# Kernel optimization log

Measured on AMD Instinct MI355X. Metric: run time of the kernel, lower is better.

The kernel has to match this reference:

```python
import jax, jax.numpy as jnp
import numpy as np

B, S, N, HID = 4, 512, 128, 64


def setup_inputs() -> dict:
    key = jax.random.key(0)
    ks = jax.random.split(key, 32)
    def rn(k, shape, scale=0.1):
        return jax.random.normal(k, shape, dtype=jnp.float32) * scale
    adj = jax.random.randint(ks[0], (N, N), 0, 2).astype(jnp.int32)
    adj = adj.at[jnp.arange(N), jnp.arange(N)].set(1)  # self loops
    inp = {
        'x': jax.random.normal(ks[1], (B, S, N, 1), dtype=jnp.float32),
        'adj': adj,
        'emb_w': rn(ks[2], (1, 16)), 'emb_b': jnp.zeros((16,), jnp.float32),
        'gat1_W': rn(ks[3], (16, 16)), 'gat1_a': rn(ks[4], (32, 1)),
        'gat2_W': rn(ks[5], (16, 8)), 'gat2_a': rn(ks[6], (16, 1)),
        'Wih0': rn(ks[7], (4 * HID, N)), 'Whh0': rn(ks[8], (4 * HID, HID)),
        'bih0': jnp.zeros((4 * HID,), jnp.float32), 'bhh0': jnp.zeros((4 * HID,), jnp.float32),
        'Wih1': rn(ks[9], (4 * HID, HID)), 'Whh1': rn(ks[10], (4 * HID, HID)),
        'bih1': jnp.zeros((4 * HID,), jnp.float32), 'bhh1': jnp.zeros((4 * HID,), jnp.float32),
    }
    comb = HID + 8 * N
    for i, name in enumerate(['dir', 'ret', 'vol']):
        o = 2 if name == 'vol' else 1
        inp[name + '_w1'] = rn(ks[11 + 4 * i], (comb, 32))
        inp[name + '_b1'] = jnp.zeros((32,), jnp.float32)
        inp[name + '_w2'] = rn(ks[12 + 4 * i], (32, o))
        inp[name + '_b2'] = jnp.zeros((o,), jnp.float32)
    return inp


def _gat(h, W, a, mask):
    # e_ij = leakyrelu(a1 . Wh_i + a2 . Wh_j): avoid torch's [M,N,N,2F] concat.
    Wh = h @ W                                  # [M, N, F]
    Fo = W.shape[1]
    f1 = Wh @ a[:Fo]                            # [M, N, 1]
    f2 = Wh @ a[Fo:]                            # [M, N, 1]
    e = jax.nn.leaky_relu(f1 + jnp.swapaxes(f2, 1, 2), 0.2)  # [M, N, N]
    e = jnp.where(mask, e, jnp.float32(-9e15))
    attn = jax.nn.softmax(e, axis=2)
    return attn @ Wh                            # [M, N, F]


def _lstm_layer(xs, Wih, Whh, bih, bhh):
    # xs: [S, B, I]; PyTorch gate order i, f, g, o
    Bsz = xs.shape[1]
    Hd = Whh.shape[1]
    def step(carry, xt):
        h, c = carry
        g = xt @ Wih.T + h @ Whh.T + bih + bhh
        i, f, gg, o = jnp.split(g, 4, axis=-1)
        c = jax.nn.sigmoid(f) * c + jax.nn.sigmoid(i) * jnp.tanh(gg)
        h = jax.nn.sigmoid(o) * jnp.tanh(c)
        return (h, c), h
    init = (jnp.zeros((Bsz, Hd), xs.dtype), jnp.zeros((Bsz, Hd), xs.dtype))
    _, hs = jax.lax.scan(step, init, xs)
    return hs


def reference(x, adj, emb_w, emb_b, gat1_W, gat1_a, gat2_W, gat2_a,
              Wih0, Whh0, bih0, bhh0, Wih1, Whh1, bih1, bhh1,
              dir_w1, dir_b1, dir_w2, dir_b2,
              ret_w1, ret_b1, ret_w2, ret_b2,
              vol_w1, vol_b1, vol_w2, vol_b2):
    Bz, Sz, Nz, _ = x.shape
    mask = (adj > 0)[None]                      # [1, N, N], broadcast over B*S
    xe = (x @ emb_w + emb_b).reshape(Bz * Sz, Nz, 16)
    xg = jax.nn.elu(_gat(xe, gat1_W, gat1_a, mask))   # gat1 concat=True -> elu
    xg = _gat(xg, gat2_W, gat2_a, mask)               # gat2 concat=False
    xg_out = xg.reshape(Bz, Sz, Nz * 8)[:, -1, :]
    xs = jnp.swapaxes(x.reshape(Bz, Sz, Nz), 0, 1)    # [S, B, N]
    hs = _lstm_layer(xs, Wih0, Whh0, bih0, bhh0)
    hs = _lstm_layer(hs, Wih1, Whh1, bih1, bhh1)      # inter-layer dropout off (eval)
    xl_out = hs[-1]                                   # [B, 64]
    c = jnp.concatenate([xl_out, xg_out], axis=1)     # [B, 64 + 8N]
    def head(w1, b1, w2, b2):
        return jax.nn.relu(c @ w1 + b1) @ w2 + b2
    return (head(dir_w1, dir_b1, dir_w2, dir_b2),
            head(ret_w1, ret_b1, ret_w2, ret_b2),
            head(vol_w1, vol_b1, vol_w2, vol_b2))
```

## Files before the change

kernel.cpp:

```cpp
#include <hip/hip_runtime.h>

#define SEQ   512
#define BATCH 4
#define NN    128
#define HID   64
#define G4    256

__device__ __forceinline__ float frcp(float x)  { return __builtin_amdgcn_rcpf(x); }
__device__ __forceinline__ float fsigm(float x) { return frcp(1.f + __expf(-x)); }
__device__ __forceinline__ float ftanh(float x) { return 1.f - 2.f * frcp(1.f + __expf(2.f * x)); }
__device__ __forceinline__ float lrelu(float x) { return x > 0.f ? x : 0.2f * x; }
__device__ __forceinline__ float dot4f(float4 w, float4 h) {
  return fmaf(w.x, h.x, fmaf(w.y, h.y, fmaf(w.z, h.z, w.w * h.w)));
}
__device__ __forceinline__ void pin4(float4& v) {
  asm volatile("" : "+v"(v.x), "+v"(v.y), "+v"(v.z), "+v"(v.w));
}
__device__ __forceinline__ float qsum(float x) {
  x += __int_as_float(__builtin_amdgcn_update_dpp(
      0, __float_as_int(x), 0xB1, 0xF, 0xF, true));
  x += __int_as_float(__builtin_amdgcn_update_dpp(
      0, __float_as_int(x), 0x4E, 0xF, 0xF, true));
  return x;
}
__device__ __forceinline__ float dotacc(const float4* w, const float4* h, float a) {
#pragma unroll
  for (int c = 0; c < 4; ++c) {
    a = fmaf(w[c].x, h[c].x, a);
    a = fmaf(w[c].y, h[c].y, a);
    a = fmaf(w[c].z, h[c].z, a);
    a = fmaf(w[c].w, h[c].w, a);
  }
  return a;
}

__global__ __launch_bounds__(512) void prep_kernel(
    const float* __restrict__ x, const float* __restrict__ Wih0,
    const float* __restrict__ bih0, const float* __restrict__ bhh0,
    float* __restrict__ X0,
    const int* __restrict__ adj, const float* __restrict__ emb_w,
    const float* __restrict__ emb_b,
    const float* __restrict__ W1, const float* __restrict__ a1,
    const float* __restrict__ W2, const float* __restrict__ a2,
    float* __restrict__ xg_out)
{
  const int tid = threadIdx.x;
  if (blockIdx.x < 128) {
    __shared__ __align__(16) float xls[NN];
    const int g = tid >> 1, half = tid & 1;
    float4 w4[16];
    {
      const float4* wp = reinterpret_cast<const float4*>(Wih0 + g * NN + half * 64);
#pragma unroll
      for (int i = 0; i < 16; ++i) w4[i] = wp[i];
    }
    const float bsum = bih0[g] + bhh0[g];
    const int r0 = blockIdx.x * 16;
    for (int r = r0; r < r0 + 16; ++r) {
      const int tt = r >> 2, b = r & 3;
      if (tid < NN) xls[tid] = x[(b * SEQ + tt) * NN + tid];
      __syncthreads();
      const float4* hp = reinterpret_cast<const float4*>(&xls[half * 64]);
      float p0 = 0.f, p1 = 0.f, p2 = 0.f, p3 = 0.f;
#pragma unroll
      for (int k = 0; k < 16; k += 4) {
        p0 += dot4f(w4[k],     hp[k]);
        p1 += dot4f(w4[k + 1], hp[k + 1]);
        p2 += dot4f(w4[k + 2], hp[k + 2]);
        p3 += dot4f(w4[k + 3], hp[k + 3]);
      }
      float p = (p0 + p1) + (p2 + p3);
      p += __shfl_xor(p, 1);
      if (half == 0) X0[r * G4 + (g & 63) * 4 + (g >> 6)] = p + bsum;
      __syncthreads();
    }
    return;
  }
  const int b = blockIdx.x - 128;
  __shared__ float adjm[NN * 129];
  __shared__ __align__(16) float xls[NN];
  __shared__ float u[16], v[16];
  __shared__ float Wh2[NN][9];
  __shared__ float f1b[NN], f2b[NN];
  __shared__ float p[NN];

  for (int idx = tid; idx < NN * NN; idx += 512)
    adjm[(idx >> 7) * 129 + (idx & 127)] = (adj[idx] > 0) ? 1.f : 0.f;
  if (tid < NN) xls[tid] = x[(b * SEQ + (SEQ - 1)) * NN + tid];
  if (tid < 16) {
    float uu = 0.f, vv = 0.f;
    for (int fp = 0; fp < 16; ++fp) {
      uu += emb_w[fp] * W1[fp * 16 + tid];
      vv += emb_b[fp] * W1[fp * 16 + tid];
    }
    u[tid] = uu; v[tid] = vv;
  }
  __syncthreads();
  float s1 = 0.f, t1 = 0.f, s2 = 0.f, t2 = 0.f;
  for (int f = 0; f < 16; ++f) {
    s1 += u[f] * a1[f];      t1 += v[f] * a1[f];
    s2 += u[f] * a1[16 + f]; t2 += v[f] * a1[16 + f];
  }
  if (tid < NN) {
    const int i = tid;
    const float f1i = xls[i] * s1 + t1;
    float m = -1e30f;
    for (int j = 0; j < NN; ++j)
      if (adjm[i * 129 + j] != 0.f)
        m = fmaxf(m, lrelu(f1i + xls[j] * s2 + t2));
    float ssum = 0.f, ps = 0.f;
    for (int j = 0; j < NN; ++j)
      if (adjm[i * 129 + j] != 0.f) {
        const float wgt = __expf(lrelu(f1i + xls[j] * s2 + t2) - m);
        ssum += wgt; ps += wgt * xls[j];
      }
    p[i] = ps / ssum;
  }
  __syncthreads();
  if (tid < NN) {
    const int i = tid;
    float xg1[16];
#pragma unroll
    for (int f = 0; f < 16; ++f) {
      const float ov = p[i] * u[f] + v[f];
      xg1[f] = ov > 0.f ? ov : expm1f(ov);
    }
    float wrow[8];
#pragma unroll
    for (int f2 = 0; f2 < 8; ++f2) wrow[f2] = 0.f;
#pragma unroll
    for (int f = 0; f < 16; ++f) {
      const float xv = xg1[f];
#pragma unroll
      for (int f2 = 0; f2 < 8; ++f2) wrow[f2] += xv * W2[f * 8 + f2];
    }
    float fb1 = 0.f, fb2 = 0.f;
#pragma unroll
    for (int f2 = 0; f2 < 8; ++f2) {
      Wh2[i][f2] = wrow[f2];
      fb1 += wrow[f2] * a2[f2];
      fb2 += wrow[f2] * a2[8 + f2];
    }
    f1b[i] = fb1; f2b[i] = fb2;
  }
  __syncthreads();
  if (tid < NN) {
    const int i = tid;
    const float fi = f1b[i];
    float m = -1e30f;
    for (int j = 0; j < NN; ++j)
      if (adjm[i * 129 + j] != 0.f)
        m = fmaxf(m, lrelu(fi + f2b[j]));
    float ssum = 0.f;
    float o[8];
#pragma unroll
    for (int f2 = 0; f2 < 8; ++f2) o[f2] = 0.f;
    for (int j = 0; j < NN; ++j)
      if (adjm[i * 129 + j] != 0.f) {
        const float wgt = __expf(lrelu(fi + f2b[j]) - m);
        ssum += wgt;
#pragma unroll
        for (int f2 = 0; f2 < 8; ++f2) o[f2] += wgt * Wh2[j][f2];
      }
    const float inv = 1.f / ssum;
#pragma unroll
    for (int f2 = 0; f2 < 8; ++f2)
      xg_out[b * (NN * 8) + i * 8 + f2] = o[f2] * inv;
  }
}

__global__ __attribute__((amdgpu_flat_work_group_size(768, 768),
                          amdgpu_waves_per_eu(3, 3)))
void lstm_heads(
    const float* __restrict__ X0T, const float* __restrict__ Whh0,
    const float* __restrict__ Wih1, const float* __restrict__ Whh1,
    const float* __restrict__ bih1, const float* __restrict__ bhh1,
    const float* __restrict__ xg,
    const float* __restrict__ dw1, const float* __restrict__ db1,
    const float* __restrict__ dw2, const float* __restrict__ db2,
    const float* __restrict__ rw1, const float* __restrict__ rb1,
    const float* __restrict__ rw2, const float* __restrict__ rb2,
    const float* __restrict__ vw1, const float* __restrict__ vb1,
    const float* __restrict__ vw2, const float* __restrict__ vb2,
    float* __restrict__ out)
{
  const int b   = blockIdx.x;
  const int t   = threadIdx.x;
  const int grp = t >> 8;
  const int r   = t & 255;
  const int uu  = r >> 2, q2 = r & 3;

  __shared__ __align__(16) float hb[2][2][HID];
  __shared__ __align__(16) float P1[2][G4];
  __shared__ float cbuf[1088];
  __shared__ float hidc[96];

  const float* Wsrc = (grp == 0) ? Whh0 : (grp == 1) ? Wih1 : Whh1;
  float4 w[4][4];
#pragma unroll
  for (int j = 0; j < 4; ++j) {
    const int row = (uu + 64 * j) * HID + 16 * q2;
#pragma unroll
    for (int c = 0; c < 4; ++c)
      w[j][c] = *reinterpret_cast<const float4*>(Wsrc + row + 4 * c);
    pin4(w[j][0]); pin4(w[j][1]); pin4(w[j][2]); pin4(w[j][3]);
  }
  float4 b1v = make_float4(0.f, 0.f, 0.f, 0.f);
  if (grp == 2) {
    b1v.x = bih1[uu]       + bhh1[uu];
    b1v.y = bih1[uu + 64]  + bhh1[uu + 64];
    b1v.z = bih1[uu + 128] + bhh1[uu + 128];
    b1v.w = bih1[uu + 192] + bhh1[uu + 192];
  }

  if (t < 256) reinterpret_cast<float*>(hb)[t] = 0.f;
  float cst = 0.f;
  const float* X0b = X0T + b * G4 + uu * 4;
  float4 cur = make_float4(0.f, 0.f, 0.f, 0.f);
  if (grp == 0) cur = *reinterpret_cast<const float4*>(X0b);
  __syncthreads();

#define LSTM_STEP(TT, RB, WB)                                                  \
  do {                                                                         \
    const float4* hp = reinterpret_cast<const float4*>(                        \
        (grp == 2) ? &hb[RB][1][0] : &hb[RB][0][0]);                           \
    float4 hq[4];                                                              \
    hq[0] = hp[4 * q2 + 0]; hq[1] = hp[4 * q2 + 1];                            \
    hq[2] = hp[4 * q2 + 2]; hq[3] = hp[4 * q2 + 3];                            \
    float4 p1v = make_float4(0.f, 0.f, 0.f, 0.f);                              \
    if (grp == 2) p1v = *reinterpret_cast<const float4*>(&P1[1 - (RB)][uu * 4]); \
    float4 nxt = cur;                                                          \
    if (grp == 0 && (TT) + 1 < SEQ)                                            \
      nxt = *reinterpret_cast<const float4*>(X0b + ((TT) + 1) * (BATCH * G4)); \
    float A0 = dotacc(w[0], hq, 0.f);                                          \
    float A1 = dotacc(w[1], hq, 0.f);                                          \
    float A2 = dotacc(w[2], hq, 0.f);                                          \
    float A3 = dotacc(w[3], hq, 0.f);                                          \
    const float S0 = qsum(A0), S1 = qsum(A1), S2 = qsum(A2), S3 = qsum(A3);    \
    if (grp == 0) {                                                            \
      if ((TT) < SEQ) {                                                        \
        const float gi = fsigm(S0 + cur.x);                                    \
        const float gf = fsigm(S1 + cur.y);                                    \
        const float gg = ftanh(S2 + cur.z);                                    \
        const float go = fsigm(S3 + cur.w);                                    \
        cst = fmaf(gf, cst, gi * gg);                                          \
        if (q2 == 0) hb[WB][0][uu] = go * ftanh(cst);                          \
      }                                                                        \
    } else if (grp == 1) {                                                     \
      if ((TT) >= 1 && (TT) <= SEQ) {                                          \
        const float sel = (q2 == 0) ? S0 : (q2 == 1) ? S1 : (q2 == 2) ? S2 : S3; \
        P1[RB][r] = sel;                                                       \
      }                                                                        \
    } else {                                                                   \
      if ((TT) >= 2) {                                                         \
        const float gi = fsigm(S0 + p1v.x + b1v.x);                            \
        const float gf = fsigm(S1 + p1v.y + b1v.y);                            \
        const float gg = ftanh(S2 + p1v.z + b1v.z);                            \
        const float go = fsigm(S3 + p1v.w + b1v.w);                            \
        cst = fmaf(gf, cst, gi * gg);                                          \
        if (q2 == 0) hb[WB][1][uu] = go * ftanh(cst);                          \
      }                                                                        \
    }                                                                          \
    cur = nxt;                                                                 \
    __syncthreads();                                                           \
  } while (0)

  for (int tt = 0; tt < SEQ + 2; tt += 2) {
    LSTM_STEP(tt, 0, 1);
    LSTM_STEP(tt + 1, 1, 0);
  }
#undef LSTM_STEP

  if (t < 64) cbuf[t] = hb[0][1][t];
  for (int k = t; k < 1024; k += 768) cbuf[64 + k] = xg[b * 1024 + k];
  __syncthreads();
  if (t < 96) {
    const int head = t >> 5, h = t & 31;
    const float* w1 = (head == 0) ? dw1 : (head == 1) ? rw1 : vw1;
    const float* b1 = (head == 0) ? db1 : (head == 1) ? rb1 : vb1;
    float a0 = 0.f, a1v = 0.f, a2v = 0.f, a3v = 0.f;
    for (int k = 0; k < 1088; k += 4) {
      a0  = fmaf(cbuf[k],     w1[k * 32 + h],       a0);
      a1v = fmaf(cbuf[k + 1], w1[(k + 1) * 32 + h], a1v);
      a2v = fmaf(cbuf[k + 2], w1[(k + 2) * 32 + h], a2v);
      a3v = fmaf(cbuf[k + 3], w1[(k + 3) * 32 + h], a3v);
    }
    hidc[head * 32 + h] = fmaxf(b1[h] + ((a0 + a1v) + (a2v + a3v)), 0.f);
  }
  __syncthreads();
  if (t < 4) {
    const int head2 = (t < 2) ? t : 2;
    const int o = (t < 2) ? 0 : (t - 2);
    const int odim = (t < 2) ? 1 : 2;
    const float* w2  = (head2 == 0) ? dw2 : (head2 == 1) ? rw2 : vw2;
    const float* b2p = (head2 == 0) ? db2 : (head2 == 1) ? rb2 : vb2;
    float acc = b2p[o];
    for (int hh = 0; hh < 32; ++hh)
      acc = fmaf(hidc[head2 * 32 + hh], w2[hh * odim + o], acc);
    const int off = (t == 0) ? b : (t == 1) ? (4 + b) : (8 + 2 * b + o);
    out[off] = acc;
  }
}

extern "C" void kernel_launch(void* const* d_in, const int* in_sizes, int n_in,
                              void* d_out, int out_size, void* d_ws, size_t ws_size,
                              hipStream_t stream) {
  const float* x     = (const float*)d_in[0];
  const int*   adj   = (const int*)  d_in[1];
  const float* emb_w = (const float*)d_in[2];
  const float* emb_b = (const float*)d_in[3];
  const float* g1W   = (const float*)d_in[4];
  const float* g1a   = (const float*)d_in[5];
  const float* g2W   = (const float*)d_in[6];
  const float* g2a   = (const float*)d_in[7];
  const float* Wih0  = (const float*)d_in[8];
  const float* Whh0  = (const float*)d_in[9];
  const float* bih0  = (const float*)d_in[10];
  const float* bhh0  = (const float*)d_in[11];
  const float* Wih1  = (const float*)d_in[12];
  const float* Whh1  = (const float*)d_in[13];
  const float* bih1  = (const float*)d_in[14];
  const float* bhh1  = (const float*)d_in[15];
  const float* dw1 = (const float*)d_in[16]; const float* db1 = (const float*)d_in[17];
  const float* dw2 = (const float*)d_in[18]; const float* db2 = (const float*)d_in[19];
  const float* rw1 = (const float*)d_in[20]; const float* rb1 = (const float*)d_in[21];
  const float* rw2 = (const float*)d_in[22]; const float* rb2 = (const float*)d_in[23];
  const float* vw1 = (const float*)d_in[24]; const float* vb1 = (const float*)d_in[25];
  const float* vw2 = (const float*)d_in[26]; const float* vb2 = (const float*)d_in[27];

  float* ws = (float*)d_ws;
  float* X0 = ws;
  float* xg = ws + SEQ * BATCH * G4;
  float* out = (float*)d_out;

  hipLaunchKernelGGL(prep_kernel, dim3(132), dim3(512), 0, stream,
                     x, Wih0, bih0, bhh0, X0,
                     adj, emb_w, emb_b, g1W, g1a, g2W, g2a, xg);
  hipLaunchKernelGGL(lstm_heads, dim3(BATCH), dim3(768), 0, stream,
                     X0, Whh0, Wih1, Whh1, bih1, bhh1, xg,
                     dw1, db1, dw2, db2, rw1, rb1, rw2, rb2,
                     vw1, vb1, vw2, vb2, out);
}
```

Before: 469.6 us.

## Merge layer-1 input and recurrent projections into one thread group

```diff
diff --git a/kernel.cpp b/kernel.cpp
--- a/kernel.cpp
+++ b/kernel.cpp
@@ -169,8 +169,8 @@
   }
 }
 
-__global__ __attribute__((amdgpu_flat_work_group_size(768, 768),
-                          amdgpu_waves_per_eu(3, 3)))
+__global__ __attribute__((amdgpu_flat_work_group_size(512, 512),
+                          amdgpu_waves_per_eu(2, 2)))
 void lstm_heads(
     const float* __restrict__ X0T, const float* __restrict__ Whh0,
     const float* __restrict__ Wih1, const float* __restrict__ Whh1,
@@ -186,27 +186,29 @@
 {
   const int b   = blockIdx.x;
   const int t   = threadIdx.x;
-  const int grp = t >> 8;
+  const bool g1 = (t >= 256);
   const int r   = t & 255;
   const int uu  = r >> 2, q2 = r & 3;
 
   __shared__ __align__(16) float hb[2][2][HID];
-  __shared__ __align__(16) float P1[2][G4];
   __shared__ float cbuf[1088];
   __shared__ float hidc[96];
 
-  const float* Wsrc = (grp == 0) ? Whh0 : (grp == 1) ? Wih1 : Whh1;
-  float4 w[4][4];
+  float4 wA[4][4], wB[4][4];
 #pragma unroll
   for (int j = 0; j < 4; ++j) {
     const int row = (uu + 64 * j) * HID + 16 * q2;
 #pragma unroll
-    for (int c = 0; c < 4; ++c)
-      w[j][c] = *reinterpret_cast<const float4*>(Wsrc + row + 4 * c);
-    pin4(w[j][0]); pin4(w[j][1]); pin4(w[j][2]); pin4(w[j][3]);
+    for (int c = 0; c < 4; ++c) {
+      wA[j][c] = *reinterpret_cast<const float4*>((g1 ? Wih1 : Whh0) + row + 4 * c);
+      wB[j][c] = g1 ? *reinterpret_cast<const float4*>(Whh1 + row + 4 * c)
+                    : make_float4(0.f, 0.f, 0.f, 0.f);
+    }
+    pin4(wA[j][0]); pin4(wA[j][1]); pin4(wA[j][2]); pin4(wA[j][3]);
+    pin4(wB[j][0]); pin4(wB[j][1]); pin4(wB[j][2]); pin4(wB[j][3]);
   }
   float4 b1v = make_float4(0.f, 0.f, 0.f, 0.f);
-  if (grp == 2) {
+  if (g1) {
     b1v.x = bih1[uu]       + bhh1[uu];
     b1v.y = bih1[uu + 64]  + bhh1[uu + 64];
     b1v.z = bih1[uu + 128] + bhh1[uu + 128];
@@ -217,27 +219,35 @@
   float cst = 0.f;
   const float* X0b = X0T + b * G4 + uu * 4;
   float4 cur = make_float4(0.f, 0.f, 0.f, 0.f);
-  if (grp == 0) cur = *reinterpret_cast<const float4*>(X0b);
+  if (!g1) cur = *reinterpret_cast<const float4*>(X0b);
   __syncthreads();
 
 #define LSTM_STEP(TT, RB, WB)                                                  \
   do {                                                                         \
-    const float4* hp = reinterpret_cast<const float4*>(                        \
-        (grp == 2) ? &hb[RB][1][0] : &hb[RB][0][0]);                           \
-    float4 hq[4];                                                              \
-    hq[0] = hp[4 * q2 + 0]; hq[1] = hp[4 * q2 + 1];                            \
-    hq[2] = hp[4 * q2 + 2]; hq[3] = hp[4 * q2 + 3];                            \
-    float4 p1v = make_float4(0.f, 0.f, 0.f, 0.f);                              \
-    if (grp == 2) p1v = *reinterpret_cast<const float4*>(&P1[1 - (RB)][uu * 4]); \
+    const float4* hp0 = reinterpret_cast<const float4*>(&hb[RB][0][0]);        \
+    const float4* hp1 = reinterpret_cast<const float4*>(&hb[RB][1][0]);        \
+    float4 hq0[4], hq1[4];                                                     \
+    hq0[0] = hp0[4 * q2 + 0]; hq0[1] = hp0[4 * q2 + 1];                        \
+    hq0[2] = hp0[4 * q2 + 2]; hq0[3] = hp0[4 * q2 + 3];                        \
+    if (g1) {                                                                  \
+      hq1[0] = hp1[4 * q2 + 0]; hq1[1] = hp1[4 * q2 + 1];                      \
+      hq1[2] = hp1[4 * q2 + 2]; hq1[3] = hp1[4 * q2 + 3];                      \
+    }                                                                          \
     float4 nxt = cur;                                                          \
-    if (grp == 0 && (TT) + 1 < SEQ)                                            \
+    if (!g1 && (TT) + 1 < SEQ)                                                 \
       nxt = *reinterpret_cast<const float4*>(X0b + ((TT) + 1) * (BATCH * G4)); \
-    float A0 = dotacc(w[0], hq, 0.f);                                          \
-    float A1 = dotacc(w[1], hq, 0.f);                                          \
-    float A2 = dotacc(w[2], hq, 0.f);                                          \
-    float A3 = dotacc(w[3], hq, 0.f);                                          \
+    float A0 = dotacc(wA[0], hq0, 0.f);                                        \
+    float A1 = dotacc(wA[1], hq0, 0.f);                                        \
+    float A2 = dotacc(wA[2], hq0, 0.f);                                        \
+    float A3 = dotacc(wA[3], hq0, 0.f);                                        \
+    if (g1) {                                                                  \
+      A0 = dotacc(wB[0], hq1, A0);                                             \
+      A1 = dotacc(wB[1], hq1, A1);                                             \
+      A2 = dotacc(wB[2], hq1, A2);                                             \
+      A3 = dotacc(wB[3], hq1, A3);                                             \
+    }                                                                          \
     const float S0 = qsum(A0), S1 = qsum(A1), S2 = qsum(A2), S3 = qsum(A3);    \
-    if (grp == 0) {                                                            \
+    if (!g1) {                                                                 \
       if ((TT) < SEQ) {                                                        \
         const float gi = fsigm(S0 + cur.x);                                    \
         const float gf = fsigm(S1 + cur.y);                                    \
@@ -246,17 +256,12 @@
         cst = fmaf(gf, cst, gi * gg);                                          \
         if (q2 == 0) hb[WB][0][uu] = go * ftanh(cst);                          \
       }                                                                        \
-    } else if (grp == 1) {                                                     \
+    } else {                                                                   \
       if ((TT) >= 1 && (TT) <= SEQ) {                                          \
-        const float sel = (q2 == 0) ? S0 : (q2 == 1) ? S1 : (q2 == 2) ? S2 : S3; \
-        P1[RB][r] = sel;                                                       \
-      }                                                                        \
-    } else {                                                                   \
-      if ((TT) >= 2) {                                                         \
-        const float gi = fsigm(S0 + p1v.x + b1v.x);                            \
-        const float gf = fsigm(S1 + p1v.y + b1v.y);                            \
-        const float gg = ftanh(S2 + p1v.z + b1v.z);                            \
-        const float go = fsigm(S3 + p1v.w + b1v.w);                            \
+        const float gi = fsigm(S0 + b1v.x);                                    \
+        const float gf = fsigm(S1 + b1v.y);                                    \
+        const float gg = ftanh(S2 + b1v.z);                                    \
+        const float go = fsigm(S3 + b1v.w);                                    \
         cst = fmaf(gf, cst, gi * gg);                                          \
         if (q2 == 0) hb[WB][1][uu] = go * ftanh(cst);                          \
       }                                                                        \
@@ -271,8 +276,8 @@
   }
 #undef LSTM_STEP
 
-  if (t < 64) cbuf[t] = hb[0][1][t];
-  for (int k = t; k < 1024; k += 768) cbuf[64 + k] = xg[b * 1024 + k];
+  if (t < 64) cbuf[t] = hb[1][1][t];
+  for (int k = t; k < 1024; k += 512) cbuf[64 + k] = xg[b * 1024 + k];
   __syncthreads();
   if (t < 96) {
     const int head = t >> 5, h = t & 31;
@@ -336,7 +341,7 @@
   hipLaunchKernelGGL(prep_kernel, dim3(132), dim3(512), 0, stream,
                      x, Wih0, bih0, bhh0, X0,
                      adj, emb_w, emb_b, g1W, g1a, g2W, g2a, xg);
-  hipLaunchKernelGGL(lstm_heads, dim3(BATCH), dim3(768), 0, stream,
+  hipLaunchKernelGGL(lstm_heads, dim3(BATCH), dim3(512), 0, stream,
                      X0, Whh0, Wih1, Whh1, bih1, bhh1, xg,
                      dw1, db1, dw2, db2, rw1, rb1, rw2, rb2,
                      vw1, vb1, vw2, vb2, out);
```

Result: slower. 593.4 us (+26.3%).
